# Kernel tuning notes

Hardware: AMD Instinct MI355X
Metric: run time of the kernel (lower is better)

Reference implementation:

```python
import jax, jax.numpy as jnp
import numpy as np

N, E = 100000, 1600000
IN_C, HID_C, OUT_C = 128, 256, 128


def _sage_conv(x, src, dst, Wl, Wr, b, n):
    # PyG SAGEConv (mean aggr): out_i = lin_l(mean_{j->i} x_j) + lin_r(x_i) + b
    msg = jax.ops.segment_sum(x[src], dst, num_segments=n)          # [N, F]
    deg = jax.ops.segment_sum(jnp.ones((src.shape[0],), x.dtype), dst, num_segments=n)
    mean = msg / jnp.maximum(deg, 1.0)[:, None]
    return mean @ Wl.T + x @ Wr.T + b


def setup_inputs() -> dict:
    key = jax.random.key(0)
    ks = jax.random.split(key, 9)
    x = jax.random.normal(ks[0], (N, IN_C), dtype=jnp.float32)
    edge_index = jax.random.randint(ks[1], (2, E), 0, N, dtype=jnp.int64)
    edge_attr = jax.random.normal(ks[2], (E, 1), dtype=jnp.float32)

    def glorot(k, fan_out, fan_in):
        s = np.sqrt(6.0 / (fan_in + fan_out)).astype(np.float32)
        return jax.random.uniform(k, (fan_out, fan_in), jnp.float32, -s, s)

    return {
        "x": x,
        "edge_index": edge_index,
        "edge_attr": edge_attr,
        "W1l": glorot(ks[3], HID_C, IN_C),
        "W1r": glorot(ks[4], HID_C, IN_C),
        "b1": jnp.zeros((HID_C,), jnp.float32),
        "W2l": glorot(ks[5], OUT_C, HID_C),
        "W2r": glorot(ks[6], OUT_C, HID_C),
        "b2": jnp.zeros((OUT_C,), jnp.float32),
    }


def reference(x, edge_index, edge_attr, W1l, W1r, b1, W2l, W2r, b2):
    src, dst = edge_index[0], edge_index[1]
    n = x.shape[0]
    h = _sage_conv(x, src, dst, W1l, W1r, b1, n)   # conv1
    h = jax.nn.relu(h)
    out = _sage_conv(h, src, dst, W2l, W2r, b2, n)  # conv2
    return out
```

## Files before the change

kernel.cpp:

```cpp
#include <hip/hip_runtime.h>


#define NBMAX 1024
#define BCAP  2560

using f32x4 = __attribute__((ext_vector_type(4))) float;
using u32x4 = __attribute__((ext_vector_type(4))) unsigned;
using u16x4 = __attribute__((ext_vector_type(4))) unsigned short;
using s16x8 = __attribute__((ext_vector_type(8))) short;
using s16x2 = __attribute__((ext_vector_type(2))) short;

#define QSCALE 15.875f

__device__ inline unsigned short f2bf(float f) {
    unsigned int u = __float_as_uint(f);
    unsigned int r = u + 0x7fff + ((u >> 16) & 1);
    return (unsigned short)(r >> 16);
}
__device__ inline float bflo(unsigned u) { return __uint_as_float(u << 16); }
__device__ inline float bfhi(unsigned u) { return __uint_as_float(u & 0xffff0000u); }

__global__ __launch_bounds__(1024) void init_kernel(int* __restrict__ bcursor,
                                                    unsigned* __restrict__ xqz,
                                                    unsigned* __restrict__ tqz, int NB) {
    int t = threadIdx.x;
    if (t < NB) bcursor[t] = t * BCAP;
    if (t < 32) xqz[t] = 0x80808080u;
    else if (t < 64) tqz[t - 32] = 0x80808080u;
}

__global__ __launch_bounds__(1024) void bin_kernel(const int* __restrict__ srci,
                                                   const int* __restrict__ dsti,
                                                   int* __restrict__ bcursor,
                                                   unsigned* __restrict__ pairs, int E, int NB) {
    __shared__ int lh[NBMAX];
    __shared__ int lbase[NBMAX];
    for (int i = threadIdx.x; i < NB; i += 1024) lh[i] = 0;
    __syncthreads();
    int chunk = (E + gridDim.x - 1) / gridDim.x;
    int e0 = blockIdx.x * chunk;
    int e1 = min(e0 + chunk, E);
    for (int e = e0 + threadIdx.x; e < e1; e += 1024)
        atomicAdd(&lh[dsti[e] >> 7], 1);
    __syncthreads();
    for (int i = threadIdx.x; i < NB; i += 1024) {
        int c = lh[i];
        lbase[i] = c ? atomicAdd(&bcursor[i], c) : 0;
        lh[i] = 0;
    }
    __syncthreads();
    for (int e = e0 + threadIdx.x; e < e1; e += 1024) {
        int d = dsti[e];
        int bk = d >> 7;
        int pos = lbase[bk] + atomicAdd(&lh[bk], 1);
        pairs[pos] = ((unsigned)srci[e] << 7) | (unsigned)(d & 127);
    }
}

__global__ __launch_bounds__(256) void csr_build_kernel(const unsigned* __restrict__ pairs,
                                                        const int* __restrict__ bcursor,
                                                        int2* __restrict__ offs2,
                                                        int* __restrict__ csr, int n) {
    __shared__ int ldeg[128];
    __shared__ int s[128];
    __shared__ int lcur[128];
    int b = blockIdx.x, tid = threadIdx.x;
    int lo = b * BCAP, hi = bcursor[b];
    if (tid < 128) ldeg[tid] = 0;
    __syncthreads();
    for (int i = lo + tid; i < hi; i += 256)
        atomicAdd(&ldeg[pairs[i] & 127], 1);
    __syncthreads();
    if (tid < 128) s[tid] = ldeg[tid];
    __syncthreads();
    for (int d = 1; d < 128; d <<= 1) {
        int add = (tid < 128 && tid >= d) ? s[tid - d] : 0;
        __syncthreads();
        if (tid < 128) s[tid] += add;
        __syncthreads();
    }
    if (tid < 128) {
        int excl = lo + s[tid] - ldeg[tid];
        int node = b * 128 + tid;
        if (node < n) offs2[node] = make_int2(excl, excl + ldeg[tid]);
        lcur[tid] = excl;
    }
    __syncthreads();
    for (int i = lo + tid; i < hi; i += 256) {
        unsigned p = pairs[i];
        int pos = atomicAdd(&lcur[p & 127], 1);
        csr[pos] = (int)(p & ~127u);
    }
}

__global__ __launch_bounds__(256) void cvt_kernel(const float* __restrict__ x,
                                                  unsigned short* __restrict__ xb,
                                                  unsigned char* __restrict__ xq, int total4,
                                                  const float* __restrict__ W1l,
                                                  const float* __restrict__ W1r,
                                                  const float* __restrict__ W2l,
                                                  const float* __restrict__ W2r,
                                                  unsigned short* __restrict__ Wb1,
                                                  unsigned short* __restrict__ Wb2l,
                                                  unsigned short* __restrict__ Wb2r) {
    if (blockIdx.x < 128) {
        for (int k = threadIdx.x; k < 1024; k += 256) {
            int idx = blockIdx.x * 1024 + k;
            int which = idx >> 15;
            int r = idx & 32767;
            if (which == 0) {
                int o = r >> 7, kk = r & 127;
                Wb1[o * 256 + kk] = f2bf(W1l[r]);
            } else if (which == 1) {
                int o = r >> 7, kk = r & 127;
                Wb1[o * 256 + 128 + kk] = f2bf(W1r[r]);
            } else if (which == 2) {
                Wb2l[r] = f2bf(W2l[r]);
            } else {
                Wb2r[r] = f2bf(W2r[r]);
            }
        }
    }
    int i = blockIdx.x * 256 + threadIdx.x;
    int stride = gridDim.x * 256;
    for (; i < total4; i += stride) {
        f32x4 v = __builtin_nontemporal_load((const f32x4*)x + i);
        u16x4 o;
        o.x = f2bf(v.x); o.y = f2bf(v.y); o.z = f2bf(v.z); o.w = f2bf(v.w);
        __builtin_nontemporal_store(o, (u16x4*)xb + i);
        int q0 = max(-127, min(127, (int)rintf(v.x * QSCALE))) + 128;
        int q1 = max(-127, min(127, (int)rintf(v.y * QSCALE))) + 128;
        int q2 = max(-127, min(127, (int)rintf(v.z * QSCALE))) + 128;
        int q3 = max(-127, min(127, (int)rintf(v.w * QSCALE))) + 128;
        unsigned qo = (unsigned)q0 | ((unsigned)q1 << 8) |
                      ((unsigned)q2 << 16) | ((unsigned)q3 << 24);
        __builtin_nontemporal_store(qo, (unsigned*)xq + i);
    }
}

template <bool OUT_F32>
__global__ __launch_bounds__(256) void agg_i8_kernel(const unsigned char* __restrict__ featq,
                                                     const int* __restrict__ csr,
                                                     const int2* __restrict__ offs2,
                                                     const unsigned short* __restrict__ uadd,
                                                     void* __restrict__ outp,
                                                     int n, int zoff, float dq) {
    int wave = threadIdx.x >> 6;
    int lane = threadIdx.x & 63;
    int slot = lane >> 3;
    int c16 = lane & 7;

    for (int base = blockIdx.x * 4; base < n; base += gridDim.x * 4) {
        int node = base + wave;
        if (node >= n) continue;
        int2 se = offs2[node];
        int start = se.x, end = se.y;
        int deg = end - start;

        s16x2 accE[4], accO[4];
#pragma unroll
        for (int j = 0; j < 4; ++j) { accE[j] = (s16x2){0, 0}; accO[j] = (s16x2){0, 0}; }

        auto addrow = [&](u32x4 v) {
#pragma unroll
            for (int j = 0; j < 4; ++j) {
                unsigned u = v[j];
                accE[j] += __builtin_bit_cast(s16x2, __builtin_amdgcn_perm(0u, u, 0x0C020C00u));
                accO[j] += __builtin_bit_cast(s16x2, __builtin_amdgcn_perm(0u, u, 0x0C030C01u));
            }
        };

        int nfull = deg >> 4;
        int e = start + slot;
        for (int it = 0; it < nfull; ++it, e += 16) {
            int o0 = csr[e];
            int o1 = csr[e + 8];
            u32x4 v0 = *(const u32x4*)(featq + (size_t)(unsigned)o0 + c16 * 16);
            u32x4 v1 = *(const u32x4*)(featq + (size_t)(unsigned)o1 + c16 * 16);
            addrow(v0);
            addrow(v1);
        }
        int done = start + (nfull << 4);
        int ntot = nfull << 4;
        if (done < end) {
            int se0 = done + slot;
            int se1 = done + 8 + slot;
            int o0 = (se0 < end) ? csr[se0] : zoff;
            int o1 = (se1 < end) ? csr[se1] : zoff;
            u32x4 v0 = *(const u32x4*)(featq + (size_t)(unsigned)o0 + c16 * 16);
            u32x4 v1 = *(const u32x4*)(featq + (size_t)(unsigned)o1 + c16 * 16);
            addrow(v0);
            addrow(v1);
            ntot += 16;
        }

#pragma unroll
        for (int m = 8; m <= 32; m <<= 1) {
#pragma unroll
            for (int j = 0; j < 4; ++j) {
                accE[j] += __builtin_bit_cast(s16x2, __shfl_xor(__builtin_bit_cast(int, accE[j]), m));
                accO[j] += __builtin_bit_cast(s16x2, __shfl_xor(__builtin_bit_cast(int, accO[j]), m));
            }
        }

        if (lane < 8) {
            float inv = dq / (float)max(deg, 1);
            float corr = 128.f * (float)ntot;
            if (OUT_F32) {
                const u32x4* up = (const u32x4*)(uadd + (size_t)node * 128 + c16 * 16);
                u32x4 ua = __builtin_nontemporal_load(up);
                u32x4 ub = __builtin_nontemporal_load(up + 1);
                unsigned uw[8] = {ua.x, ua.y, ua.z, ua.w, ub.x, ub.y, ub.z, ub.w};
                float* dst = (float*)outp + (size_t)node * 128 + c16 * 16;
#pragma unroll
                for (int j = 0; j < 4; ++j) {
                    f32x4 fv;
                    fv[0] = ((float)accE[j][0] - corr) * inv + bflo(uw[2 * j]);
                    fv[1] = ((float)accO[j][0] - corr) * inv + bfhi(uw[2 * j]);
                    fv[2] = ((float)accE[j][1] - corr) * inv + bflo(uw[2 * j + 1]);
                    fv[3] = ((float)accO[j][1] - corr) * inv + bfhi(uw[2 * j + 1]);
                    __builtin_nontemporal_store(fv, (f32x4*)(dst + 4 * j));
                }
            } else {
                unsigned wbuf[8];
#pragma unroll
                for (int j = 0; j < 4; ++j) {
                    float f0 = ((float)accE[j][0] - corr) * inv;
                    float f1 = ((float)accO[j][0] - corr) * inv;
                    float f2 = ((float)accE[j][1] - corr) * inv;
                    float f3 = ((float)accO[j][1] - corr) * inv;
                    wbuf[2 * j]     = (unsigned)f2bf(f0) | ((unsigned)f2bf(f1) << 16);
                    wbuf[2 * j + 1] = (unsigned)f2bf(f2) | ((unsigned)f2bf(f3) << 16);
                }
                u32x4* dst = (u32x4*)((unsigned short*)outp + (size_t)node * 128 + c16 * 16);
                u32x4 w0 = {wbuf[0], wbuf[1], wbuf[2], wbuf[3]};
                u32x4 w1 = {wbuf[4], wbuf[5], wbuf[6], wbuf[7]};
                __builtin_nontemporal_store(w0, dst);
                __builtin_nontemporal_store(w1, dst + 1);
            }
        }
    }
}

template <int OSTRIDE, int EPI>
__global__ __launch_bounds__(256) void gemm_persist_kernel(
    const unsigned short* __restrict__ A0, const unsigned short* __restrict__ A1,
    const unsigned short* __restrict__ Wb, const float* __restrict__ bias,
    void* __restrict__ outv, int n, int ntiles) {
    __shared__ unsigned short As[2][32 * 256];
    const int tid = threadIdx.x;
    const int w = tid >> 6, lane = tid & 63;
    const int l15 = lane & 15, lhi = lane >> 4;
    const int colbase = blockIdx.y * 128 + w * 32;

    s16x8 b[8][2];
#pragma unroll
    for (int kk = 0; kk < 8; ++kk)
#pragma unroll
        for (int cf = 0; cf < 2; ++cf)
            b[kk][cf] = *(const s16x8*)(Wb + (size_t)(colbase + cf * 16 + l15) * 256 +
                                        kk * 32 + lhi * 8);

    s16x8 st[4];
    auto stage_load = [&](int tile) {
#pragma unroll
        for (int p = 0; p < 4; ++p) {
            int chunk = p * 256 + tid;
            int row = chunk >> 5;
            int cc = chunk & 31;
            int grow = tile * 32 + row;
            if (grow >= n) grow = n - 1;
            const unsigned short* src;
            if (A1) {
                src = (cc < 16) ? (A0 + (size_t)grow * 128 + cc * 8)
                                : (A1 + (size_t)grow * 128 + (cc - 16) * 8);
            } else {
                src = A0 + (size_t)grow * 256 + cc * 8;
            }
            st[p] = *(const s16x8*)src;
        }
    };
    auto stage_write = [&](int buf) {
#pragma unroll
        for (int p = 0; p < 4; ++p) {
            int chunk = p * 256 + tid;
            int row = chunk >> 5;
            int cc = chunk & 31;
            int scc = (cc & 24) | ((cc ^ (row & 7)) & 7);
            *(s16x8*)((char*)&As[buf][0] + row * 512 + scc * 16) = st[p];
        }
    };

    int t = blockIdx.x;
    if (t >= ntiles) return;
    stage_load(t);
    stage_write(0);
    __syncthreads();
    int buf = 0;

    for (; t < ntiles; t += gridDim.x) {
        int tn = t + gridDim.x;
        bool hasNext = tn < ntiles;
        if (hasNext) stage_load(tn);

        f32x4 acc[2][2];
#pragma unroll
        for (int rf = 0; rf < 2; ++rf)
#pragma unroll
            for (int cf = 0; cf < 2; ++cf)
                acc[rf][cf] = (f32x4){0.f, 0.f, 0.f, 0.f};

#pragma unroll
        for (int kk = 0; kk < 8; ++kk) {
            s16x8 a[2];
#pragma unroll
            for (int rf = 0; rf < 2; ++rf) {
                int row = rf * 16 + l15;
                int cbase = kk * 4 + lhi;
                int scc = (cbase & 24) | ((cbase ^ (row & 7)) & 7);
                a[rf] = *(const s16x8*)((const char*)&As[buf][0] + row * 512 + scc * 16);
            }
#pragma unroll
            for (int rf = 0; rf < 2; ++rf)
#pragma unroll
                for (int cf = 0; cf < 2; ++cf)
                    acc[rf][cf] = __builtin_amdgcn_mfma_f32_16x16x32_bf16(
                        b[kk][cf], a[rf], acc[rf][cf], 0, 0, 0);
        }

        __syncthreads();
        if (hasNext) stage_write(buf ^ 1);
        __syncthreads();

#pragma unroll
        for (int rf = 0; rf < 2; ++rf) {
            int row = t * 32 + rf * 16 + l15;
            if (row >= n) continue;
#pragma unroll
            for (int cf = 0; cf < 2; ++cf) {
                int colg = colbase + cf * 16 + lhi * 4;
                f32x4 v = acc[rf][cf];
                float4 bb = *(const float4*)(bias + colg);
                v[0] += bb.x; v[1] += bb.y; v[2] += bb.z; v[3] += bb.w;
                if (EPI == 1) {
                    v[0] = fmaxf(v[0], 0.f); v[1] = fmaxf(v[1], 0.f);
                    v[2] = fmaxf(v[2], 0.f); v[3] = fmaxf(v[3], 0.f);
                }
                uint2 o;
                o.x = (unsigned)f2bf(v[0]) | ((unsigned)f2bf(v[1]) << 16);
                o.y = (unsigned)f2bf(v[2]) | ((unsigned)f2bf(v[3]) << 16);
                *(uint2*)((unsigned short*)outv + (size_t)row * OSTRIDE + colg) = o;
            }
        }
        buf ^= 1;
    }
}

__global__ __launch_bounds__(256, 2) void gemm_dual_kernel(
    const unsigned short* __restrict__ A0,
    const unsigned short* __restrict__ WbL, const unsigned short* __restrict__ WbR,
    const float* __restrict__ bias,
    unsigned char* __restrict__ tq, unsigned short* __restrict__ u,
    int n, int ntiles) {
    __shared__ unsigned short As[2][32 * 256];
    const int tid = threadIdx.x;
    const int w = tid >> 6, lane = tid & 63;
    const int l15 = lane & 15, lhi = lane >> 4;
    const int colbase = w * 32;

    s16x8 bL[8][2], bR[8][2];
#pragma unroll
    for (int kk = 0; kk < 8; ++kk)
#pragma unroll
        for (int cf = 0; cf < 2; ++cf) {
            size_t off = (size_t)(colbase + cf * 16 + l15) * 256 + kk * 32 + lhi * 8;
            bL[kk][cf] = *(const s16x8*)(WbL + off);
            bR[kk][cf] = *(const s16x8*)(WbR + off);
        }

    s16x8 st[4];
    auto stage_load = [&](int tile) {
#pragma unroll
        for (int p = 0; p < 4; ++p) {
            int chunk = p * 256 + tid;
            int row = chunk >> 5;
            int cc = chunk & 31;
            int grow = tile * 32 + row;
            if (grow >= n) grow = n - 1;
            st[p] = *(const s16x8*)(A0 + (size_t)grow * 256 + cc * 8);
        }
    };
    auto stage_write = [&](int buf) {
#pragma unroll
        for (int p = 0; p < 4; ++p) {
            int chunk = p * 256 + tid;
            int row = chunk >> 5;
            int cc = chunk & 31;
            int scc = (cc & 24) | ((cc ^ (row & 7)) & 7);
            *(s16x8*)((char*)&As[buf][0] + row * 512 + scc * 16) = st[p];
        }
    };

    int t = blockIdx.x;
    if (t >= ntiles) return;
    stage_load(t);
    stage_write(0);
    __syncthreads();
    int buf = 0;

    for (; t < ntiles; t += gridDim.x) {
        int tn = t + gridDim.x;
        bool hasNext = tn < ntiles;
        if (hasNext) stage_load(tn);

        f32x4 accL[2][2], accR[2][2];
#pragma unroll
        for (int rf = 0; rf < 2; ++rf)
#pragma unroll
            for (int cf = 0; cf < 2; ++cf) {
                accL[rf][cf] = (f32x4){0.f, 0.f, 0.f, 0.f};
                accR[rf][cf] = (f32x4){0.f, 0.f, 0.f, 0.f};
            }

#pragma unroll
        for (int kk = 0; kk < 8; ++kk) {
            s16x8 a[2];
#pragma unroll
            for (int rf = 0; rf < 2; ++rf) {
                int row = rf * 16 + l15;
                int cbase = kk * 4 + lhi;
                int scc = (cbase & 24) | ((cbase ^ (row & 7)) & 7);
                a[rf] = *(const s16x8*)((const char*)&As[buf][0] + row * 512 + scc * 16);
            }
#pragma unroll
            for (int rf = 0; rf < 2; ++rf)
#pragma unroll
                for (int cf = 0; cf < 2; ++cf) {
                    accL[rf][cf] = __builtin_amdgcn_mfma_f32_16x16x32_bf16(
                        bL[kk][cf], a[rf], accL[rf][cf], 0, 0, 0);
                    accR[rf][cf] = __builtin_amdgcn_mfma_f32_16x16x32_bf16(
                        bR[kk][cf], a[rf], accR[rf][cf], 0, 0, 0);
                }
        }

        __syncthreads();
        if (hasNext) stage_write(buf ^ 1);
        __syncthreads();

#pragma unroll
        for (int rf = 0; rf < 2; ++rf) {
            int row = t * 32 + rf * 16 + l15;
            if (row >= n) continue;
#pragma unroll
            for (int cf = 0; cf < 2; ++cf) {
                int colg = colbase + cf * 16 + lhi * 4;
                f32x4 vL = accL[rf][cf];
                int q0 = max(-127, min(127, (int)rintf(vL[0] * QSCALE))) + 128;
                int q1 = max(-127, min(127, (int)rintf(vL[1] * QSCALE))) + 128;
                int q2 = max(-127, min(127, (int)rintf(vL[2] * QSCALE))) + 128;
                int q3 = max(-127, min(127, (int)rintf(vL[3] * QSCALE))) + 128;
                unsigned oq = (unsigned)q0 | ((unsigned)q1 << 8) |
                              ((unsigned)q2 << 16) | ((unsigned)q3 << 24);
                *(unsigned*)(tq + (size_t)row * 128 + colg) = oq;
                f32x4 vR = accR[rf][cf];
                float4 bb = *(const float4*)(bias + colg);
                vR[0] += bb.x; vR[1] += bb.y; vR[2] += bb.z; vR[3] += bb.w;
                uint2 ou;
                ou.x = (unsigned)f2bf(vR[0]) | ((unsigned)f2bf(vR[1]) << 16);
                ou.y = (unsigned)f2bf(vR[2]) | ((unsigned)f2bf(vR[3]) << 16);
                *(uint2*)(u + (size_t)row * 128 + colg) = ou;
            }
        }
        buf ^= 1;
    }
}

extern "C" void kernel_launch(void* const* d_in, const int* in_sizes, int n_in,
                              void* d_out, int out_size, void* d_ws, size_t ws_size,
                              hipStream_t stream) {
    const float* x   = (const float*)d_in[0];
    const int*   ei  = (const int*)d_in[1];
    const float* W1l = (const float*)d_in[3];
    const float* W1r = (const float*)d_in[4];
    const float* b1  = (const float*)d_in[5];
    const float* W2l = (const float*)d_in[6];
    const float* W2r = (const float*)d_in[7];
    const float* b2  = (const float*)d_in[8];

    const int n = in_sizes[0] / 128;
    const int E = in_sizes[1] / 2;
    const int* srci = ei;
    const int* dsti = ei + E;
    const int NB = (n + 127) >> 7;

    char* w = (char*)d_ws;
    auto alloc = [&](size_t bytes) {
        char* p = w;
        w += (bytes + 255) & ~(size_t)255;
        return p;
    };
    int*      bcursor = (int*)alloc((size_t)NBMAX * 4);
    int2*     offs2   = (int2*)alloc((size_t)n * 8);
    unsigned* pairs   = (unsigned*)alloc((size_t)NB * BCAP * 4);
    int*      csr     = (int*)alloc((size_t)NB * BCAP * 4);
    unsigned short* Wb1   = (unsigned short*)alloc((size_t)256 * 256 * 2);
    unsigned short* Wb2l  = (unsigned short*)alloc((size_t)128 * 256 * 2);
    unsigned short* Wb2r  = (unsigned short*)alloc((size_t)128 * 256 * 2);
    unsigned short* xb    = (unsigned short*)alloc((size_t)n * 128 * 2);
    unsigned char*  xq    = (unsigned char*)alloc((size_t)(n + 1) * 128);
    unsigned short* mean1b= (unsigned short*)alloc((size_t)n * 128 * 2);
    unsigned short* hb    = (unsigned short*)alloc((size_t)n * 256 * 2);
    unsigned char*  tq    = (unsigned char*)alloc((size_t)(n + 1) * 128);
    float*          outp  = (float*)d_out;

    init_kernel<<<1, 1024, 0, stream>>>(bcursor, (unsigned*)(xq + (size_t)n * 128),
                                        (unsigned*)(tq + (size_t)n * 128), NB);
    bin_kernel<<<256, 1024, 0, stream>>>(srci, dsti, bcursor, pairs, E, NB);
    csr_build_kernel<<<NB, 256, 0, stream>>>(pairs, bcursor, offs2, csr, n);
    cvt_kernel<<<2048, 256, 0, stream>>>(x, xb, xq, n * 128 / 4,
                                         W1l, W1r, W2l, W2r, Wb1, Wb2l, Wb2r);

    const int ntiles = (n + 31) / 32;
    const int zoff = n * 128;
    const float dq = 1.f / QSCALE;
    agg_i8_kernel<false><<<2048, 256, 0, stream>>>(xq, csr, offs2, nullptr, mean1b, n, zoff, dq);
    gemm_persist_kernel<256, 1><<<dim3(768, 2), 256, 0, stream>>>(mean1b, xb, Wb1, b1, hb, n, ntiles);
    gemm_dual_kernel<<<512, 256, 0, stream>>>(hb, Wb2l, Wb2r, b2, tq, mean1b, n, ntiles);
    agg_i8_kernel<true><<<2048, 256, 0, stream>>>(tq, csr, offs2, mean1b, outp, n, zoff, dq);
}
```

Before: 217.0 us.

## Fuse binning with conversion kernel and launch one aggregation block per four nodes

Result: faster. 208.9 us, median of 3 (-3.7%).

```diff
diff --git a/kernel.cpp b/kernel.cpp
--- a/kernel.cpp
+++ b/kernel.cpp
@@ -6,7 +6,6 @@
 
 using f32x4 = __attribute__((ext_vector_type(4))) float;
 using u32x4 = __attribute__((ext_vector_type(4))) unsigned;
-using u16x4 = __attribute__((ext_vector_type(4))) unsigned short;
 using s16x8 = __attribute__((ext_vector_type(8))) short;
 using s16x2 = __attribute__((ext_vector_type(2))) short;
 
@@ -29,31 +28,70 @@
     else if (t < 64) tqz[t - 32] = 0x80808080u;
 }
 
-__global__ __launch_bounds__(1024) void bin_kernel(const int* __restrict__ srci,
-                                                   const int* __restrict__ dsti,
-                                                   int* __restrict__ bcursor,
-                                                   unsigned* __restrict__ pairs, int E, int NB) {
+__global__ __launch_bounds__(1024) void bin_cvt_kernel(
+    const int* __restrict__ srci, const int* __restrict__ dsti,
+    int* __restrict__ bcursor, unsigned* __restrict__ pairs, int E, int NB,
+    const float* __restrict__ x, unsigned short* __restrict__ xb,
+    unsigned char* __restrict__ xq, int total4,
+    const float* __restrict__ W1l, const float* __restrict__ W1r,
+    const float* __restrict__ W2l, const float* __restrict__ W2r,
+    unsigned short* __restrict__ Wb1, unsigned short* __restrict__ Wb2l,
+    unsigned short* __restrict__ Wb2r) {
     __shared__ int lh[NBMAX];
     __shared__ int lbase[NBMAX];
-    for (int i = threadIdx.x; i < NB; i += 1024) lh[i] = 0;
-    __syncthreads();
-    int chunk = (E + gridDim.x - 1) / gridDim.x;
-    int e0 = blockIdx.x * chunk;
-    int e1 = min(e0 + chunk, E);
-    for (int e = e0 + threadIdx.x; e < e1; e += 1024)
-        atomicAdd(&lh[dsti[e] >> 7], 1);
-    __syncthreads();
-    for (int i = threadIdx.x; i < NB; i += 1024) {
-        int c = lh[i];
-        lbase[i] = c ? atomicAdd(&bcursor[i], c) : 0;
-        lh[i] = 0;
-    }
-    __syncthreads();
-    for (int e = e0 + threadIdx.x; e < e1; e += 1024) {
-        int d = dsti[e];
-        int bk = d >> 7;
-        int pos = lbase[bk] + atomicAdd(&lh[bk], 1);
-        pairs[pos] = ((unsigned)srci[e] << 7) | (unsigned)(d & 127);
+    if (blockIdx.x < 256) {
+        for (int i = threadIdx.x; i < NB; i += 1024) lh[i] = 0;
+        __syncthreads();
+        int chunk = (E + 255) / 256;
+        int e0 = blockIdx.x * chunk;
+        int e1 = min(e0 + chunk, E);
+        for (int e = e0 + threadIdx.x; e < e1; e += 1024)
+            atomicAdd(&lh[dsti[e] >> 7], 1);
+        __syncthreads();
+        for (int i = threadIdx.x; i < NB; i += 1024) {
+            int c = lh[i];
+            lbase[i] = c ? atomicAdd(&bcursor[i], c) : 0;
+            lh[i] = 0;
+        }
+        __syncthreads();
+        for (int e = e0 + threadIdx.x; e < e1; e += 1024) {
+            int d = dsti[e];
+            int bk = d >> 7;
+            int pos = lbase[bk] + atomicAdd(&lh[bk], 1);
+            pairs[pos] = ((unsigned)srci[e] << 7) | (unsigned)(d & 127);
+        }
+        return;
+    }
+    int cvtid = blockIdx.x - 256;
+    if (cvtid < 128) {
+        int idx = cvtid * 1024 + threadIdx.x;
+        int which = idx >> 15;
+        int r = idx & 32767;
+        if (which == 0) {
+            int o = r >> 7, kk = r & 127;
+            Wb1[o * 256 + kk] = f2bf(W1l[r]);
+        } else if (which == 1) {
+            int o = r >> 7, kk = r & 127;
+            Wb1[o * 256 + 128 + kk] = f2bf(W1r[r]);
+        } else if (which == 2) {
+            Wb2l[r] = f2bf(W2l[r]);
+        } else {
+            Wb2r[r] = f2bf(W2r[r]);
+        }
+    }
+    int i = cvtid * 1024 + threadIdx.x;
+    int stride = 1024 * 1024;
+    for (; i < total4; i += stride) {
+        float4 v = ((const float4*)x)[i];
+        ushort4 o;
+        o.x = f2bf(v.x); o.y = f2bf(v.y); o.z = f2bf(v.z); o.w = f2bf(v.w);
+        ((ushort4*)xb)[i] = o;
+        int q0 = max(-127, min(127, (int)rintf(v.x * QSCALE))) + 128;
+        int q1 = max(-127, min(127, (int)rintf(v.y * QSCALE))) + 128;
+        int q2 = max(-127, min(127, (int)rintf(v.z * QSCALE))) + 128;
+        int q3 = max(-127, min(127, (int)rintf(v.w * QSCALE))) + 128;
+        ((unsigned*)xq)[i] = (unsigned)q0 | ((unsigned)q1 << 8) |
+                             ((unsigned)q2 << 16) | ((unsigned)q3 << 24);
     }
 }
 
@@ -93,51 +131,6 @@
     }
 }
 
-__global__ __launch_bounds__(256) void cvt_kernel(const float* __restrict__ x,
-                                                  unsigned short* __restrict__ xb,
-                                                  unsigned char* __restrict__ xq, int total4,
-                                                  const float* __restrict__ W1l,
-                                                  const float* __restrict__ W1r,
-                                                  const float* __restrict__ W2l,
-                                                  const float* __restrict__ W2r,
-                                                  unsigned short* __restrict__ Wb1,
-                                                  unsigned short* __restrict__ Wb2l,
-                                                  unsigned short* __restrict__ Wb2r) {
-    if (blockIdx.x < 128) {
-        for (int k = threadIdx.x; k < 1024; k += 256) {
-            int idx = blockIdx.x * 1024 + k;
-            int which = idx >> 15;
-            int r = idx & 32767;
-            if (which == 0) {
-                int o = r >> 7, kk = r & 127;
-                Wb1[o * 256 + kk] = f2bf(W1l[r]);
-            } else if (which == 1) {
-                int o = r >> 7, kk = r & 127;
-                Wb1[o * 256 + 128 + kk] = f2bf(W1r[r]);
-            } else if (which == 2) {
-                Wb2l[r] = f2bf(W2l[r]);
-            } else {
-                Wb2r[r] = f2bf(W2r[r]);
-            }
-        }
-    }
-    int i = blockIdx.x * 256 + threadIdx.x;
-    int stride = gridDim.x * 256;
-    for (; i < total4; i += stride) {
-        f32x4 v = __builtin_nontemporal_load((const f32x4*)x + i);
-        u16x4 o;
-        o.x = f2bf(v.x); o.y = f2bf(v.y); o.z = f2bf(v.z); o.w = f2bf(v.w);
-        __builtin_nontemporal_store(o, (u16x4*)xb + i);
-        int q0 = max(-127, min(127, (int)rintf(v.x * QSCALE))) + 128;
-        int q1 = max(-127, min(127, (int)rintf(v.y * QSCALE))) + 128;
-        int q2 = max(-127, min(127, (int)rintf(v.z * QSCALE))) + 128;
-        int q3 = max(-127, min(127, (int)rintf(v.w * QSCALE))) + 128;
-        unsigned qo = (unsigned)q0 | ((unsigned)q1 << 8) |
-                      ((unsigned)q2 << 16) | ((unsigned)q3 << 24);
-        __builtin_nontemporal_store(qo, (unsigned*)xq + i);
-    }
-}
-
 template <bool OUT_F32>
 __global__ __launch_bounds__(256) void agg_i8_kernel(const unsigned char* __restrict__ featq,
                                                      const int* __restrict__ csr,
@@ -147,97 +140,92 @@
                                                      int n, int zoff, float dq) {
     int wave = threadIdx.x >> 6;
     int lane = threadIdx.x & 63;
+    int node = blockIdx.x * 4 + wave;
+    if (node >= n) return;
+    int2 se = offs2[node];
+    int start = se.x, end = se.y;
+    int deg = end - start;
     int slot = lane >> 3;
     int c16 = lane & 7;
 
-    for (int base = blockIdx.x * 4; base < n; base += gridDim.x * 4) {
-        int node = base + wave;
-        if (node >= n) continue;
-        int2 se = offs2[node];
-        int start = se.x, end = se.y;
-        int deg = end - start;
-
-        s16x2 accE[4], accO[4];
-#pragma unroll
-        for (int j = 0; j < 4; ++j) { accE[j] = (s16x2){0, 0}; accO[j] = (s16x2){0, 0}; }
-
-        auto addrow = [&](u32x4 v) {
+    s16x2 accE[4], accO[4];
+#pragma unroll
+    for (int j = 0; j < 4; ++j) { accE[j] = (s16x2){0, 0}; accO[j] = (s16x2){0, 0}; }
+
+    auto addrow = [&](u32x4 v) {
+#pragma unroll
+        for (int j = 0; j < 4; ++j) {
+            unsigned u = v[j];
+            accE[j] += __builtin_bit_cast(s16x2, __builtin_amdgcn_perm(0u, u, 0x0C020C00u));
+            accO[j] += __builtin_bit_cast(s16x2, __builtin_amdgcn_perm(0u, u, 0x0C030C01u));
+        }
+    };
+
+    int nfull = deg >> 4;
+    int e = start + slot;
+    for (int it = 0; it < nfull; ++it, e += 16) {
+        int o0 = csr[e];
+        int o1 = csr[e + 8];
+        u32x4 v0 = *(const u32x4*)(featq + (size_t)(unsigned)o0 + c16 * 16);
+        u32x4 v1 = *(const u32x4*)(featq + (size_t)(unsigned)o1 + c16 * 16);
+        addrow(v0);
+        addrow(v1);
+    }
+    int done = start + (nfull << 4);
+    int ntot = nfull << 4;
+    if (done < end) {
+        int se0 = done + slot;
+        int se1 = done + 8 + slot;
+        int o0 = (se0 < end) ? csr[se0] : zoff;
+        int o1 = (se1 < end) ? csr[se1] : zoff;
+        u32x4 v0 = *(const u32x4*)(featq + (size_t)(unsigned)o0 + c16 * 16);
+        u32x4 v1 = *(const u32x4*)(featq + (size_t)(unsigned)o1 + c16 * 16);
+        addrow(v0);
+        addrow(v1);
+        ntot += 16;
+    }
+
+#pragma unroll
+    for (int m = 8; m <= 32; m <<= 1) {
+#pragma unroll
+        for (int j = 0; j < 4; ++j) {
+            accE[j] += __builtin_bit_cast(s16x2, __shfl_xor(__builtin_bit_cast(int, accE[j]), m));
+            accO[j] += __builtin_bit_cast(s16x2, __shfl_xor(__builtin_bit_cast(int, accO[j]), m));
+        }
+    }
+
+    if (lane < 8) {
+        float inv = dq / (float)max(deg, 1);
+        float corr = 128.f * (float)ntot;
+        if (OUT_F32) {
+            const u32x4* up = (const u32x4*)(uadd + (size_t)node * 128 + c16 * 16);
+            u32x4 ua = up[0];
+            u32x4 ub = up[1];
+            unsigned uw[8] = {ua.x, ua.y, ua.z, ua.w, ub.x, ub.y, ub.z, ub.w};
+            float* dst = (float*)outp + (size_t)node * 128 + c16 * 16;
 #pragma unroll
             for (int j = 0; j < 4; ++j) {
-                unsigned u = v[j];
-                accE[j] += __builtin_bit_cast(s16x2, __builtin_amdgcn_perm(0u, u, 0x0C020C00u));
-                accO[j] += __builtin_bit_cast(s16x2, __builtin_amdgcn_perm(0u, u, 0x0C030C01u));
-            }
-        };
-
-        int nfull = deg >> 4;
-        int e = start + slot;
-        for (int it = 0; it < nfull; ++it, e += 16) {
-            int o0 = csr[e];
-            int o1 = csr[e + 8];
-            u32x4 v0 = *(const u32x4*)(featq + (size_t)(unsigned)o0 + c16 * 16);
-            u32x4 v1 = *(const u32x4*)(featq + (size_t)(unsigned)o1 + c16 * 16);
-            addrow(v0);
-            addrow(v1);
-        }
-        int done = start + (nfull << 4);
-        int ntot = nfull << 4;
-        if (done < end) {
-            int se0 = done + slot;
-            int se1 = done + 8 + slot;
-            int o0 = (se0 < end) ? csr[se0] : zoff;
-            int o1 = (se1 < end) ? csr[se1] : zoff;
-            u32x4 v0 = *(const u32x4*)(featq + (size_t)(unsigned)o0 + c16 * 16);
-            u32x4 v1 = *(const u32x4*)(featq + (size_t)(unsigned)o1 + c16 * 16);
-            addrow(v0);
-            addrow(v1);
-            ntot += 16;
-        }
-
-#pragma unroll
-        for (int m = 8; m <= 32; m <<= 1) {
+                f32x4 fv;
+                fv[0] = ((float)accE[j][0] - corr) * inv + bflo(uw[2 * j]);
+                fv[1] = ((float)accO[j][0] - corr) * inv + bfhi(uw[2 * j]);
+                fv[2] = ((float)accE[j][1] - corr) * inv + bflo(uw[2 * j + 1]);
+                fv[3] = ((float)accO[j][1] - corr) * inv + bfhi(uw[2 * j + 1]);
+                *(f32x4*)(dst + 4 * j) = fv;
+            }
+        } else {
+            unsigned wbuf[8];
 #pragma unroll
             for (int j = 0; j < 4; ++j) {
-                accE[j] += __builtin_bit_cast(s16x2, __shfl_xor(__builtin_bit_cast(int, accE[j]), m));
-                accO[j] += __builtin_bit_cast(s16x2, __shfl_xor(__builtin_bit_cast(int, accO[j]), m));
-            }
-        }
-
-        if (lane < 8) {
-            float inv = dq / (float)max(deg, 1);
-            float corr = 128.f * (float)ntot;
-            if (OUT_F32) {
-                const u32x4* up = (const u32x4*)(uadd + (size_t)node * 128 + c16 * 16);
-                u32x4 ua = __builtin_nontemporal_load(up);
-                u32x4 ub = __builtin_nontemporal_load(up + 1);
-                unsigned uw[8] = {ua.x, ua.y, ua.z, ua.w, ub.x, ub.y, ub.z, ub.w};
-                float* dst = (float*)outp + (size_t)node * 128 + c16 * 16;
-#pragma unroll
-                for (int j = 0; j < 4; ++j) {
-                    f32x4 fv;
-                    fv[0] = ((float)accE[j][0] - corr) * inv + bflo(uw[2 * j]);
-                    fv[1] = ((float)accO[j][0] - corr) * inv + bfhi(uw[2 * j]);
-                    fv[2] = ((float)accE[j][1] - corr) * inv + bflo(uw[2 * j + 1]);
-                    fv[3] = ((float)accO[j][1] - corr) * inv + bfhi(uw[2 * j + 1]);
-                    __builtin_nontemporal_store(fv, (f32x4*)(dst + 4 * j));
-                }
-            } else {
-                unsigned wbuf[8];
-#pragma unroll
-                for (int j = 0; j < 4; ++j) {
-                    float f0 = ((float)accE[j][0] - corr) * inv;
-                    float f1 = ((float)accO[j][0] - corr) * inv;
-                    float f2 = ((float)accE[j][1] - corr) * inv;
-                    float f3 = ((float)accO[j][1] - corr) * inv;
-                    wbuf[2 * j]     = (unsigned)f2bf(f0) | ((unsigned)f2bf(f1) << 16);
-                    wbuf[2 * j + 1] = (unsigned)f2bf(f2) | ((unsigned)f2bf(f3) << 16);
-                }
-                u32x4* dst = (u32x4*)((unsigned short*)outp + (size_t)node * 128 + c16 * 16);
-                u32x4 w0 = {wbuf[0], wbuf[1], wbuf[2], wbuf[3]};
-                u32x4 w1 = {wbuf[4], wbuf[5], wbuf[6], wbuf[7]};
-                __builtin_nontemporal_store(w0, dst);
-                __builtin_nontemporal_store(w1, dst + 1);
-            }
+                float f0 = ((float)accE[j][0] - corr) * inv;
+                float f1 = ((float)accO[j][0] - corr) * inv;
+                float f2 = ((float)accE[j][1] - corr) * inv;
+                float f3 = ((float)accO[j][1] - corr) * inv;
+                wbuf[2 * j]     = (unsigned)f2bf(f0) | ((unsigned)f2bf(f1) << 16);
+                wbuf[2 * j + 1] = (unsigned)f2bf(f2) | ((unsigned)f2bf(f3) << 16);
+            }
+            u32x4* dst = (u32x4*)((unsigned short*)outp + (size_t)node * 128 + c16 * 16);
+            dst[0] = (u32x4){wbuf[0], wbuf[1], wbuf[2], wbuf[3]};
+            dst[1] = (u32x4){wbuf[4], wbuf[5], wbuf[6], wbuf[7]};
         }
     }
 }
@@ -515,16 +503,16 @@
 
     init_kernel<<<1, 1024, 0, stream>>>(bcursor, (unsigned*)(xq + (size_t)n * 128),
                                         (unsigned*)(tq + (size_t)n * 128), NB);
-    bin_kernel<<<256, 1024, 0, stream>>>(srci, dsti, bcursor, pairs, E, NB);
+    bin_cvt_kernel<<<1280, 1024, 0, stream>>>(srci, dsti, bcursor, pairs, E, NB,
+                                              x, xb, xq, n * 128 / 4,
+                                              W1l, W1r, W2l, W2r, Wb1, Wb2l, Wb2r);
     csr_build_kernel<<<NB, 256, 0, stream>>>(pairs, bcursor, offs2, csr, n);
-    cvt_kernel<<<2048, 256, 0, stream>>>(x, xb, xq, n * 128 / 4,
-                                         W1l, W1r, W2l, W2r, Wb1, Wb2l, Wb2r);
 
     const int ntiles = (n + 31) / 32;
     const int zoff = n * 128;
     const float dq = 1.f / QSCALE;
-    agg_i8_kernel<false><<<2048, 256, 0, stream>>>(xq, csr, offs2, nullptr, mean1b, n, zoff, dq);
+    agg_i8_kernel<false><<<(n + 3) / 4, 256, 0, stream>>>(xq, csr, offs2, nullptr, mean1b, n, zoff, dq);
     gemm_persist_kernel<256, 1><<<dim3(768, 2), 256, 0, stream>>>(mean1b, xb, Wb1, b1, hb, n, ntiles);
     gemm_dual_kernel<<<512, 256, 0, stream>>>(hb, Wb2l, Wb2r, b2, tq, mean1b, n, ntiles);
-    agg_i8_kernel<true><<<2048, 256, 0, stream>>>(tq, csr, offs2, mean1b, outp, n, zoff, dq);
-}
+    agg_i8_kernel<true><<<(n + 3) / 4, 256, 0, stream>>>(tq, csr, offs2, mean1b, outp, n, zoff, dq);
+}
```
